# Kernel optimization log

Hardware: AMD Instinct MI355X
Metric: run time of the kernel (lower is better)

The kernel has to match this reference:

```python
import jax, jax.numpy as jnp
import numpy as np
import math

B, CF, H, W = 2, 64, 256, 256
CH = 32          # 'channel' init arg
KS, DIL, PAD = 3, 2, 2
IMG_H, IMG_W = 512, 512


def _pos_encode(h, w, d_model):
    # Sinusoidal encoding along x and y, interleaved sin/cos -> [2*d_model, h, w]
    div = jnp.exp(jnp.arange(0, d_model, 2, dtype=jnp.float32) * (-math.log(10000.0) / d_model))  # [d/2]
    ax = jnp.arange(w, dtype=jnp.float32)[None, :] * div[:, None]   # [d/2, w]
    ay = jnp.arange(h, dtype=jnp.float32)[None, :] * div[:, None]   # [d/2, h]
    x = jnp.stack([jnp.sin(ax), jnp.cos(ax)], axis=1).reshape(d_model, w)  # even=sin, odd=cos
    y = jnp.stack([jnp.sin(ay), jnp.cos(ay)], axis=1).reshape(d_model, h)
    x = jnp.broadcast_to(x[:, None, :], (d_model, h, w))
    y = jnp.broadcast_to(y[:, :, None], (d_model, h, w))
    return jnp.concatenate([x, y], axis=0)  # [2*d_model, h, w]


def _unfold3x3(x):
    # F.unfold(kernel=3, dilation=2, padding=2, stride=1) -> [B, C, 9, H, W]
    b, c, h, w = x.shape
    xp = jnp.pad(x, ((0, 0), (0, 0), (PAD, PAD), (PAD, PAD)))
    offs = (0, DIL, 2 * DIL)
    patches = [xp[:, :, i:i + h, j:j + w] for i in offs for j in offs]  # row-major kernel order
    return jnp.stack(patches, axis=2)


def setup_inputs() -> dict:
    key = jax.random.key(0)
    k1, k2, k3, k4, k5 = jax.random.split(key, 5)
    return {
        "inp": jax.random.normal(k1, (B, CF, H, W), dtype=jnp.float32),
        "img": jax.random.uniform(k2, (B, 3, IMG_H, IMG_W), dtype=jnp.float32),
        "w_pos": jax.random.normal(k3, (CH, 2 * CH), dtype=jnp.float32) * 0.1,
        "w_img": jax.random.normal(k4, (CH, 3), dtype=jnp.float32) * 0.1,
        "w_comp": jax.random.normal(k5, (CF,), dtype=jnp.float32) * 0.1,
    }


def reference(inp, img, w_pos, w_img, w_comp):
    b, cf, h, w = inp.shape
    # positional embedding -> 1x1 conv (channel matmul)
    pos = _pos_encode(h, w, CH)                                   # [2*CH, H, W]
    pos_embd = jnp.einsum('oc,chw->ohw', w_pos, pos)              # [CH, H, W]
    pos_embd = jnp.broadcast_to(pos_embd[None], (b, CH, h, w))
    # bilinear resize of image to feature resolution, then 1x1 conv
    rimg = jax.image.resize(img, (b, 3, h, w), method='bilinear')
    rimg = jnp.einsum('oc,bchw->bohw', w_img, rimg)               # [B, CH, H, W]
    em = jnp.concatenate([rimg, pos_embd], axis=1)                # [B, 2*CH, H, W]
    # neighborhood similarity score
    un_em = _unfold3x3(em)                                        # [B, 2CH, 9, H, W]
    feature_score = jnp.einsum('bckhw,bchw->bkhw', un_em, em)     # [B, 9, H, W]
    # feature compatibility: 1x1 conv (dot with w_comp) per neighbor, sigmoid
    un_fea = _unfold3x3(inp)                                      # [B, CF, 9, H, W]
    comp_score = jax.nn.sigmoid(jnp.einsum('bckhw,c->bkhw', un_fea, w_comp))
    phi = comp_score * feature_score                              # [B, 9, H, W]
    weighted_fea = jnp.einsum('bckhw,bkhw->bchw', un_fea, phi)    # [B, CF, H, W]
    return weighted_fea
```

## Files before the change

kernel.cpp:

```cpp
#include <hip/hip_runtime.h>
#include <math.h>

namespace {
constexpr int Bn = 2, CF = 64;
constexpr int H = 256, W = 256, HW = H * W;
constexpr int IH = 512, IW = 512;

constexpr int OFF_MT   = 0;
constexpr int OFF_GXX  = OFF_MT + 256 * 256;
constexpr int OFF_GYY  = OFF_GXX + 3 * 256;
constexpr int OFF_G    = OFF_GYY + 3 * 256;
constexpr int OFF_RIMG = OFF_G + 16;
constexpr int OFF_S    = OFF_RIMG + Bn * 3 * HW;
constexpr int OFF_PHI  = OFF_S + Bn * HW;
constexpr int OFF_PX   = OFF_RIMG;
constexpr int OFF_PY   = OFF_RIMG + 32 * 256;
}

__global__ __launch_bounds__(256) void pxy_kernel(
    const float* __restrict__ w_pos,
    float* __restrict__ PX, float* __restrict__ PY)
{
  const int t = threadIdx.x;
  const int o = blockIdx.x;
  float s[16], c[16];
#pragma unroll
  for (int i = 0; i < 16; i++) {
    float d = expf((float)(2 * i) * (-0.2878231366242557f));
    float a = (float)t * d;
    s[i] = sinf(a);
    c[i] = cosf(a);
  }
  const float* wr = w_pos + o * 64;
  float ax = 0.f, ay = 0.f;
#pragma unroll
  for (int i = 0; i < 16; i++) {
    ax += wr[2 * i] * s[i] + wr[2 * i + 1] * c[i];
    ay += wr[32 + 2 * i] * s[i] + wr[33 + 2 * i] * c[i];
  }
  PX[o * 256 + t] = ax;
  PY[o * 256 + t] = ay;
}

__global__ __launch_bounds__(256) void gram_kernel(
    const float* __restrict__ PX, const float* __restrict__ PY,
    const float* __restrict__ w_img,
    float* __restrict__ Mt, float* __restrict__ GXX, float* __restrict__ GYY,
    float* __restrict__ G)
{
  const int a = threadIdx.x;
  const int t = blockIdx.x;

  float m = 0.f;
#pragma unroll
  for (int o = 0; o < 32; o++) m += PX[o * 256 + a] * PY[o * 256 + t];
  Mt[t * 256 + a] = m;

  if (t == 0) {
#pragma unroll
    for (int j = 0; j < 3; j++) {
      const int nb = a + 2 * (j - 1);
      float gx = 0.f, gy = 0.f;
      if (nb >= 0 && nb < 256) {
#pragma unroll
        for (int o = 0; o < 32; o++) {
          gx += PX[o * 256 + a] * PX[o * 256 + nb];
          gy += PY[o * 256 + a] * PY[o * 256 + nb];
        }
      }
      GXX[j * 256 + a] = gx;
      GYY[j * 256 + a] = gy;
    }
    if (a < 9) {
      const int i = a / 3, j = a % 3;
      float g = 0.f;
#pragma unroll
      for (int o = 0; o < 32; o++) g += w_img[o * 3 + i] * w_img[o * 3 + j];
      G[a] = g;
    }
  }
}

__device__ __forceinline__ void resize_taps(int p, int n, float w[4], int idx[4])
{
#pragma unroll
  for (int r = 0; r < 4; r++) {
    int q = 2 * p - 1 + r;
    idx[r] = min(max(q, 0), 2 * n - 1);
  }
  if (p == 0)          { w[0] = 0.f;        w[1] = 3.f / 7.f; w[2] = 3.f / 7.f; w[3] = 1.f / 7.f; }
  else if (p == n - 1) { w[0] = 1.f / 7.f;  w[1] = 3.f / 7.f; w[2] = 3.f / 7.f; w[3] = 0.f; }
  else                 { w[0] = 0.125f;     w[1] = 0.375f;    w[2] = 0.375f;    w[3] = 0.125f; }
}

__global__ __launch_bounds__(256) void rimg_kernel(
    const float* __restrict__ img, float* __restrict__ rimg)
{
  const int p = blockIdx.x * 256 + threadIdx.x;
  const int c = blockIdx.y;
  const int b = blockIdx.z;
  const int x = p & (W - 1);
  const int y = p >> 8;

  float wy[4], wx[4];
  int ry[4], rx[4];
  resize_taps(y, H, wy, ry);
  resize_taps(x, W, wx, rx);

  const float* ip = img + ((size_t)(b * 3 + c) * IH) * IW;
  float acc = 0.f;
#pragma unroll
  for (int r = 0; r < 4; r++) {
    const float* rowp = ip + ry[r] * IW;
    float rs = wx[0] * rowp[rx[0]] + wx[1] * rowp[rx[1]] +
               wx[2] * rowp[rx[2]] + wx[3] * rowp[rx[3]];
    acc += wy[r] * rs;
  }
  rimg[((size_t)(b * 3 + c)) * HW + p] = acc;
}

__global__ __launch_bounds__(256) void smap_kernel(
    const float* __restrict__ inp, const float* __restrict__ w_comp,
    float* __restrict__ smap)
{
  __shared__ float red[256];
  const int lane = threadIdx.x & 63;
  const int cg = threadIdx.x >> 6;
  const int p = blockIdx.x * 64 + lane;
  const int b = blockIdx.z;

  const float* ib = inp + (size_t)b * CF * HW + (size_t)cg * 16 * HW + p;
  float a0 = 0.f, a1 = 0.f, a2 = 0.f, a3 = 0.f;
#pragma unroll
  for (int c = 0; c < 16; c += 4) {
    a0 += ib[(size_t)(c + 0) * HW] * w_comp[cg * 16 + c + 0];
    a1 += ib[(size_t)(c + 1) * HW] * w_comp[cg * 16 + c + 1];
    a2 += ib[(size_t)(c + 2) * HW] * w_comp[cg * 16 + c + 2];
    a3 += ib[(size_t)(c + 3) * HW] * w_comp[cg * 16 + c + 3];
  }
  red[threadIdx.x] = (a0 + a1) + (a2 + a3);
  __syncthreads();
  if (threadIdx.x < 64) {
    smap[(size_t)b * HW + blockIdx.x * 64 + threadIdx.x] =
        red[threadIdx.x] + red[threadIdx.x + 64] +
        red[threadIdx.x + 128] + red[threadIdx.x + 192];
  }
}

__global__ __launch_bounds__(256) void phi_kernel(
    const float* __restrict__ rimg, const float* __restrict__ smap,
    const float* __restrict__ Mt, const float* __restrict__ GXX,
    const float* __restrict__ GYY, const float* __restrict__ G,
    float* __restrict__ phi)
{
  const int p = blockIdx.x * 256 + threadIdx.x;
  const int k = blockIdx.y;
  const int b = blockIdx.z;
  const int x = p & (W - 1);
  const int y = p >> 8;
  const int ky = k / 3, kx = k % 3;
  const int ny = y + 2 * (ky - 1), nx = x + 2 * (kx - 1);
  const bool valid = ((unsigned)ny < (unsigned)H) & ((unsigned)nx < (unsigned)W);
  const int cy = min(max(ny, 0), H - 1);
  const int cx = min(max(nx, 0), W - 1);
  const int np = cy * W + cx;

  const float* rb = rimg + (size_t)b * 3 * HW;
  const float r0 = rb[p],            r1 = rb[HW + p],      r2 = rb[2 * HW + p];
  const float n0 = rb[np],           n1 = rb[HW + np],     n2 = rb[2 * HW + np];

  const float g0 = G[0], g1 = G[1], g2 = G[2];
  const float g3 = G[3], g4 = G[4], g5 = G[5];
  const float g6 = G[6], g7 = G[7], g8 = G[8];

  float fs = r0 * (g0 * n0 + g1 * n1 + g2 * n2)
           + r1 * (g3 * n0 + g4 * n1 + g5 * n2)
           + r2 * (g6 * n0 + g7 * n1 + g8 * n2);
  fs += GXX[kx * 256 + x] + GYY[ky * 256 + y] + Mt[y * 256 + cx] + Mt[cy * 256 + x];

  const float s = smap[(size_t)b * HW + np];
  const float cs = 1.f / (1.f + expf(-s));
  phi[((size_t)(b * 9 + k)) * HW + p] = valid ? cs * fs : 0.f;
}

__global__ __launch_bounds__(256) void gather_kernel(
    const float* __restrict__ inp, const float* __restrict__ phi,
    float* __restrict__ out)
{
  const int cg = blockIdx.x;
  const int p = blockIdx.y * 256 + threadIdx.x;
  const int b = blockIdx.z;
  const int x = p & (W - 1);
  const int y = p >> 8;

  float ph[9];
  int nb[9];
#pragma unroll
  for (int k = 0; k < 9; k++) {
    const int ky = k / 3, kx = k % 3;
    const int ny = y + 2 * (ky - 1), nx = x + 2 * (kx - 1);
    const int cy = min(max(ny, 0), H - 1);
    const int cx = min(max(nx, 0), W - 1);
    nb[k] = cy * W + cx;
    ph[k] = phi[((size_t)(b * 9 + k)) * HW + p];
  }

  const float* ib = inp + (size_t)b * CF * HW + (size_t)cg * 4 * HW;
  float* ob = out + (size_t)b * CF * HW + (size_t)cg * 4 * HW;
#pragma unroll
  for (int c = 0; c < 4; c++) {
    const float* ic = ib + (size_t)c * HW;
    float acc = ph[0] * ic[nb[0]];
#pragma unroll
    for (int k = 1; k < 9; k++) acc += ph[k] * ic[nb[k]];
    ob[(size_t)c * HW + p] = acc;
  }
}

extern "C" void kernel_launch(void* const* d_in, const int* in_sizes, int n_in,
                              void* d_out, int out_size, void* d_ws, size_t ws_size,
                              hipStream_t stream)
{
  const float* inp    = (const float*)d_in[0];
  const float* img    = (const float*)d_in[1];
  const float* w_pos  = (const float*)d_in[2];
  const float* w_img  = (const float*)d_in[3];
  const float* w_comp = (const float*)d_in[4];
  float* out = (float*)d_out;
  float* ws  = (float*)d_ws;

  float* Mt   = ws + OFF_MT;
  float* GXX  = ws + OFF_GXX;
  float* GYY  = ws + OFF_GYY;
  float* G    = ws + OFF_G;
  float* rimg = ws + OFF_RIMG;
  float* smap = ws + OFF_S;
  float* phi  = ws + OFF_PHI;
  float* PX   = ws + OFF_PX;
  float* PY   = ws + OFF_PY;

  hipLaunchKernelGGL(pxy_kernel, dim3(32), dim3(256), 0, stream, w_pos, PX, PY);
  hipLaunchKernelGGL(gram_kernel, dim3(256), dim3(256), 0, stream,
                     PX, PY, w_img, Mt, GXX, GYY, G);

  hipLaunchKernelGGL(rimg_kernel, dim3(HW / 256, 3, Bn), dim3(256), 0, stream,
                     img, rimg);
  hipLaunchKernelGGL(smap_kernel, dim3(HW / 64, 1, Bn), dim3(256), 0, stream,
                     inp, w_comp, smap);

  hipLaunchKernelGGL(phi_kernel, dim3(HW / 256, 9, Bn), dim3(256), 0, stream,
                     rimg, smap, Mt, GXX, GYY, G, phi);

  hipLaunchKernelGGL(gather_kernel, dim3(CF / 4, HW / 256, Bn), dim3(256), 0, stream,
                     inp, phi, out);
}
```

Measured before the change: 125.1 us.

## Fuse phi computation into gather kernel and merge positional-encoding kernels

Folds the phi computation into the gather kernel, so the 9 neighbour weights are computed in registers instead of being written to and read back from a global phi buffer. Each block now handles 16 channels rather than 4, which amortises the recomputation of phi across more channels. It also merges pxy and gram into one kernel that keeps PX/PY in shared memory, with every block recomputing them redundantly. This removes two launches and the phi round trip, at the cost of fewer, heavier blocks and redundant positional-encoding work.

```diff
diff --git a/kernel.cpp b/kernel.cpp
--- a/kernel.cpp
+++ b/kernel.cpp
@@ -12,17 +12,18 @@
 constexpr int OFF_G    = OFF_GYY + 3 * 256;
 constexpr int OFF_RIMG = OFF_G + 16;
 constexpr int OFF_S    = OFF_RIMG + Bn * 3 * HW;
-constexpr int OFF_PHI  = OFF_S + Bn * HW;
-constexpr int OFF_PX   = OFF_RIMG;
-constexpr int OFF_PY   = OFF_RIMG + 32 * 256;
-}
-
-__global__ __launch_bounds__(256) void pxy_kernel(
-    const float* __restrict__ w_pos,
-    float* __restrict__ PX, float* __restrict__ PY)
-{
+}
+
+__global__ __launch_bounds__(256) void pos_kernel(
+    const float* __restrict__ w_pos, const float* __restrict__ w_img,
+    float* __restrict__ Mt, float* __restrict__ GXX, float* __restrict__ GYY,
+    float* __restrict__ G)
+{
+  __shared__ float PX[32][256];
+  __shared__ float PY[32][256];
   const int t = threadIdx.x;
-  const int o = blockIdx.x;
+  const int blk = blockIdx.x;
+
   float s[16], c[16];
 #pragma unroll
   for (int i = 0; i < 16; i++) {
@@ -31,52 +32,46 @@
     s[i] = sinf(a);
     c[i] = cosf(a);
   }
-  const float* wr = w_pos + o * 64;
-  float ax = 0.f, ay = 0.f;
-#pragma unroll
-  for (int i = 0; i < 16; i++) {
-    ax += wr[2 * i] * s[i] + wr[2 * i + 1] * c[i];
-    ay += wr[32 + 2 * i] * s[i] + wr[33 + 2 * i] * c[i];
-  }
-  PX[o * 256 + t] = ax;
-  PY[o * 256 + t] = ay;
-}
-
-__global__ __launch_bounds__(256) void gram_kernel(
-    const float* __restrict__ PX, const float* __restrict__ PY,
-    const float* __restrict__ w_img,
-    float* __restrict__ Mt, float* __restrict__ GXX, float* __restrict__ GYY,
-    float* __restrict__ G)
-{
-  const int a = threadIdx.x;
-  const int t = blockIdx.x;
+#pragma unroll 4
+  for (int o = 0; o < 32; o++) {
+    const float* wr = w_pos + o * 64;
+    float ax = 0.f, ay = 0.f;
+#pragma unroll
+    for (int i = 0; i < 16; i++) {
+      ax += wr[2 * i] * s[i] + wr[2 * i + 1] * c[i];
+      ay += wr[32 + 2 * i] * s[i] + wr[33 + 2 * i] * c[i];
+    }
+    PX[o][t] = ax;
+    PY[o][t] = ay;
+  }
+  __syncthreads();
 
   float m = 0.f;
 #pragma unroll
-  for (int o = 0; o < 32; o++) m += PX[o * 256 + a] * PY[o * 256 + t];
-  Mt[t * 256 + a] = m;
-
-  if (t == 0) {
+  for (int o = 0; o < 32; o++) m += PX[o][t] * PY[o][blk];
+  Mt[blk * 256 + t] = m;
+
+  if (blk == 0) {
 #pragma unroll
     for (int j = 0; j < 3; j++) {
-      const int nb = a + 2 * (j - 1);
+      const int nb = t + 2 * (j - 1);
       float gx = 0.f, gy = 0.f;
       if (nb >= 0 && nb < 256) {
 #pragma unroll
         for (int o = 0; o < 32; o++) {
-          gx += PX[o * 256 + a] * PX[o * 256 + nb];
-          gy += PY[o * 256 + a] * PY[o * 256 + nb];
+          gx += PX[o][t] * PX[o][nb];
+          gy += PY[o][t] * PY[o][nb];
         }
       }
-      GXX[j * 256 + a] = gx;
-      GYY[j * 256 + a] = gy;
+      GXX[j * 256 + t] = gx;
+      GYY[j * 256 + t] = gy;
     }
-    if (a < 9) {
-      const int i = a / 3, j = a % 3;
+    if (t < 9) {
+      const int i = t / 3, j = t % 3;
       float g = 0.f;
 #pragma unroll
       for (int o = 0; o < 32; o++) g += w_img[o * 3 + i] * w_img[o * 3 + j];
-      G[a] = g;
+      G[t] = g;
     }
   }
 }
@@ -147,45 +142,11 @@
   }
 }
 
-__global__ __launch_bounds__(256) void phi_kernel(
-    const float* __restrict__ rimg, const float* __restrict__ smap,
-    const float* __restrict__ Mt, const float* __restrict__ GXX,
-    const float* __restrict__ GYY, const float* __restrict__ G,
-    float* __restrict__ phi)
-{
-  const int p = blockIdx.x * 256 + threadIdx.x;
-  const int k = blockIdx.y;
-  const int b = blockIdx.z;
-  const int x = p & (W - 1);
-  const int y = p >> 8;
-  const int ky = k / 3, kx = k % 3;
-  const int ny = y + 2 * (ky - 1), nx = x + 2 * (kx - 1);
-  const bool valid = ((unsigned)ny < (unsigned)H) & ((unsigned)nx < (unsigned)W);
-  const int cy = min(max(ny, 0), H - 1);
-  const int cx = min(max(nx, 0), W - 1);
-  const int np = cy * W + cx;
-
-  const float* rb = rimg + (size_t)b * 3 * HW;
-  const float r0 = rb[p],            r1 = rb[HW + p],      r2 = rb[2 * HW + p];
-  const float n0 = rb[np],           n1 = rb[HW + np],     n2 = rb[2 * HW + np];
-
-  const float g0 = G[0], g1 = G[1], g2 = G[2];
-  const float g3 = G[3], g4 = G[4], g5 = G[5];
-  const float g6 = G[6], g7 = G[7], g8 = G[8];
-
-  float fs = r0 * (g0 * n0 + g1 * n1 + g2 * n2)
-           + r1 * (g3 * n0 + g4 * n1 + g5 * n2)
-           + r2 * (g6 * n0 + g7 * n1 + g8 * n2);
-  fs += GXX[kx * 256 + x] + GYY[ky * 256 + y] + Mt[y * 256 + cx] + Mt[cy * 256 + x];
-
-  const float s = smap[(size_t)b * HW + np];
-  const float cs = 1.f / (1.f + expf(-s));
-  phi[((size_t)(b * 9 + k)) * HW + p] = valid ? cs * fs : 0.f;
-}
-
-__global__ __launch_bounds__(256) void gather_kernel(
-    const float* __restrict__ inp, const float* __restrict__ phi,
-    float* __restrict__ out)
+__global__ __launch_bounds__(256) void phigather_kernel(
+    const float* __restrict__ inp, const float* __restrict__ rimg,
+    const float* __restrict__ smap, const float* __restrict__ Mt,
+    const float* __restrict__ GXX, const float* __restrict__ GYY,
+    const float* __restrict__ G, float* __restrict__ out)
 {
   const int cg = blockIdx.x;
   const int p = blockIdx.y * 256 + threadIdx.x;
@@ -193,22 +154,41 @@
   const int x = p & (W - 1);
   const int y = p >> 8;
 
+  const float* rb = rimg + (size_t)b * 3 * HW;
+  const float r0 = rb[p], r1 = rb[HW + p], r2 = rb[2 * HW + p];
+  const float g0 = G[0], g1 = G[1], g2 = G[2];
+  const float g3 = G[3], g4 = G[4], g5 = G[5];
+  const float g6 = G[6], g7 = G[7], g8 = G[8];
+  const float* sb = smap + (size_t)b * HW;
+
   float ph[9];
   int nb[9];
 #pragma unroll
   for (int k = 0; k < 9; k++) {
     const int ky = k / 3, kx = k % 3;
     const int ny = y + 2 * (ky - 1), nx = x + 2 * (kx - 1);
+    const bool valid = ((unsigned)ny < (unsigned)H) & ((unsigned)nx < (unsigned)W);
     const int cy = min(max(ny, 0), H - 1);
     const int cx = min(max(nx, 0), W - 1);
-    nb[k] = cy * W + cx;
-    ph[k] = phi[((size_t)(b * 9 + k)) * HW + p];
-  }
-
-  const float* ib = inp + (size_t)b * CF * HW + (size_t)cg * 4 * HW;
-  float* ob = out + (size_t)b * CF * HW + (size_t)cg * 4 * HW;
-#pragma unroll
-  for (int c = 0; c < 4; c++) {
+    const int np = cy * W + cx;
+    nb[k] = np;
+
+    const float n0 = rb[np], n1 = rb[HW + np], n2 = rb[2 * HW + np];
+    float fs = r0 * (g0 * n0 + g1 * n1 + g2 * n2)
+             + r1 * (g3 * n0 + g4 * n1 + g5 * n2)
+             + r2 * (g6 * n0 + g7 * n1 + g8 * n2);
+    fs += GXX[kx * 256 + x] + GYY[ky * 256 + y]
+        + Mt[y * 256 + cx] + Mt[cy * 256 + x];
+
+    const float s = sb[np];
+    const float cs = 1.f / (1.f + expf(-s));
+    ph[k] = valid ? cs * fs : 0.f;
+  }
+
+  const float* ib = inp + (size_t)b * CF * HW + (size_t)cg * 16 * HW;
+  float* ob = out + (size_t)b * CF * HW + (size_t)cg * 16 * HW;
+#pragma unroll 4
+  for (int c = 0; c < 16; c++) {
     const float* ic = ib + (size_t)c * HW;
     float acc = ph[0] * ic[nb[0]];
 #pragma unroll
@@ -235,22 +215,15 @@
   float* G    = ws + OFF_G;
   float* rimg = ws + OFF_RIMG;
   float* smap = ws + OFF_S;
-  float* phi  = ws + OFF_PHI;
-  float* PX   = ws + OFF_PX;
-  float* PY   = ws + OFF_PY;
-
-  hipLaunchKernelGGL(pxy_kernel, dim3(32), dim3(256), 0, stream, w_pos, PX, PY);
-  hipLaunchKernelGGL(gram_kernel, dim3(256), dim3(256), 0, stream,
-                     PX, PY, w_img, Mt, GXX, GYY, G);
+
+  hipLaunchKernelGGL(pos_kernel, dim3(256), dim3(256), 0, stream,
+                     w_pos, w_img, Mt, GXX, GYY, G);
 
   hipLaunchKernelGGL(rimg_kernel, dim3(HW / 256, 3, Bn), dim3(256), 0, stream,
                      img, rimg);
   hipLaunchKernelGGL(smap_kernel, dim3(HW / 64, 1, Bn), dim3(256), 0, stream,
                      inp, w_comp, smap);
 
-  hipLaunchKernelGGL(phi_kernel, dim3(HW / 256, 9, Bn), dim3(256), 0, stream,
-                     rimg, smap, Mt, GXX, GYY, G, phi);
-
-  hipLaunchKernelGGL(gather_kernel, dim3(CF / 4, HW / 256, Bn), dim3(256), 0, stream,
-                     inp, phi, out);
-}
+  hipLaunchKernelGGL(phigather_kernel, dim3(CF / 16, HW / 256, Bn), dim3(256), 0, stream,
+                     inp, rimg, smap, Mt, GXX, GYY, G, out);
+}
```

Measured after the change: 142.2 us. 1.14x slower.
